# Kernel tuning notes

Hardware: AMD Instinct MI355X
Metric: run time of the kernel (lower is better)

The kernel has to match this reference:

```python
import jax, jax.numpy as jnp
import numpy as np

B, T, DM, DK = 16, 2048, 1024, 128

def setup_inputs() -> dict:
    key = jax.random.key(0)
    k1, k2, k3, k4 = jax.random.split(key, 4)
    x = jax.random.normal(k1, (B, T, DM), dtype=jnp.float32)
    # Linear(dm, dk, bias=False) weights, stored as [dm, dk] for x @ W
    scale = 1.0 / np.sqrt(DM)
    W_q = jax.random.normal(k2, (DM, DK), dtype=jnp.float32) * scale
    W_k = jax.random.normal(k3, (DM, DK), dtype=jnp.float32) * scale
    W_v = jax.random.normal(k4, (DM, DK), dtype=jnp.float32) * scale
    return {"x": x, "W_q": W_q, "W_k": W_k, "W_v": W_v}

def reference(x, W_q, W_k, W_v):
    # q, k, v: [B, T, DK]
    q = jnp.einsum('btd,dk->btk', x, W_q)
    k = jnp.einsum('btd,dk->btk', x, W_k)
    v = jnp.einsum('btd,dk->btk', x, W_v)
    dk = k.shape[-1]
    # scores: [B, T, T], scaled by dk**-0.5
    wei = jnp.einsum('bqk,bsk->bqs', q, k) * (dk ** -0.5)
    # causal mask (tril == 0 -> -inf)
    causal = jnp.tril(jnp.ones((q.shape[1], q.shape[1]), dtype=bool))
    wei = jnp.where(causal, wei, -jnp.inf)
    wei = jax.nn.softmax(wei, axis=-1)
    out = jnp.einsum('bqs,bsk->bqk', wei, v)  # [B, T, DK]
    return out
```

## Files before the change

### kernel.cpp

```cpp
#include <hip/hip_runtime.h>
#include <hip/hip_bf16.h>

#define NB 16
#define NT 2048
#define NDM 1024
#define NDK 128

typedef __bf16 bf16;
typedef bf16 bf16x4 __attribute__((ext_vector_type(4)));
typedef bf16 bf16x8 __attribute__((ext_vector_type(8)));
typedef float f32x4 __attribute__((ext_vector_type(4)));

__device__ inline bf16 to_bf16(float f) {
    __hip_bfloat16 h = __float2bfloat16(f);
    return *reinterpret_cast<bf16*>(&h);
}

__device__ inline void gload_lds16(const void* g, void* l) {
    __builtin_amdgcn_global_load_lds(
        (const __attribute__((address_space(1))) unsigned int*)g,
        (__attribute__((address_space(3))) unsigned int*)l, 16, 0, 0);
}

__global__ __launch_bounds__(256) void transpose_w_kernel(
        const float* __restrict__ Wq, const float* __restrict__ Wk,
        const float* __restrict__ Wv, bf16* __restrict__ Wt) {
    int idx = blockIdx.x * 256 + threadIdx.x;
    int w = idx >> 17;
    int r = idx & (NDM * NDK - 1);
    int k = r >> 7;
    int n = r & (NDK - 1);
    const float* W = (w == 0) ? Wq : ((w == 1) ? Wk : Wv);
    Wt[(size_t)w * NDK * NDM + (size_t)n * NDM + k] = to_bf16(W[(size_t)k * NDK + n]);
}

__global__ __launch_bounds__(512) void proj_fused_kernel(
        const float* __restrict__ x, const bf16* __restrict__ Wt,
        bf16* __restrict__ qkv, bf16* __restrict__ Vt) {
    __shared__ __align__(16) char smem[65536];
    const int tid = threadIdx.x;
    const int lane = tid & 63, wave = tid >> 6;
    const int wr = wave >> 2, wc = wave & 3;
    const int r16 = lane & 15, kg = lane >> 4;
    const int mb = blockIdx.x;
    const float* xA = x + (size_t)mb * 128 * NDM;

    auto ASB = [&](int b) -> bf16* { return (bf16*)(smem + b * 8192); };
    auto BSB = [&](int b) -> bf16* { return (bf16*)(smem + 16384 + b * 24576); };

    const int a_row = tid >> 2, a_c = tid & 3;
    const int a_dst = (a_row * 4 + (a_c ^ ((a_row >> 1) & 3))) * 8;
    const size_t a_src = (size_t)a_row * NDM + a_c * 8;

    auto loadA = [&](int k0, float4& lo, float4& hi) {
        lo = *reinterpret_cast<const float4*>(xA + a_src + k0);
        hi = *reinterpret_cast<const float4*>(xA + a_src + k0 + 4);
    };
    auto writeA = [&](int buf, const float4& lo, const float4& hi) {
        bf16x8 v;
        v[0] = to_bf16(lo.x); v[1] = to_bf16(lo.y); v[2] = to_bf16(lo.z); v[3] = to_bf16(lo.w);
        v[4] = to_bf16(hi.x); v[5] = to_bf16(hi.y); v[6] = to_bf16(hi.z); v[7] = to_bf16(hi.w);
        *reinterpret_cast<bf16x8*>(ASB(buf) + a_dst) = v;
    };
    auto stageB = [&](int buf, int k0) {
#pragma unroll
        for (int p = 0; p < 3; p++) {
            int cid = p * 512 + tid;
            int w = cid >> 9, rem = cid & 511;
            int row = rem >> 2, c = rem & 3;
            int cs = c ^ ((row >> 1) & 3);
            gload_lds16(Wt + (size_t)w * NDK * NDM + (size_t)row * NDM + k0 + cs * 8,
                        BSB(buf) + (p * 512 + wave * 64) * 8);
        }
    };

    f32x4 acc[3][4][2];
#pragma unroll
    for (int w = 0; w < 3; w++)
#pragma unroll
        for (int m = 0; m < 4; m++)
#pragma unroll
            for (int n = 0; n < 2; n++) acc[w][m][n] = (f32x4){0.f, 0.f, 0.f, 0.f};

    {
        float4 lo, hi;
        loadA(0, lo, hi);
        writeA(0, lo, hi);
        stageB(0, 0);
    }
    __syncthreads();

    for (int kt = 0; kt < NDM / 32; kt++) {
        const int cur = kt & 1;
        const bool pf = (kt + 1 < NDM / 32);
        float4 lo, hi;
        if (pf) {
            loadA((kt + 1) * 32, lo, hi);
            stageB(1 - cur, (kt + 1) * 32);
        }

        bf16x8 af[4];
#pragma unroll
        for (int m = 0; m < 4; m++) {
            int arow = wr * 64 + m * 16 + r16;
            int ch = kg ^ ((arow >> 1) & 3);
            af[m] = *reinterpret_cast<const bf16x8*>(ASB(cur) + (arow * 4 + ch) * 8);
        }
#pragma unroll
        for (int w = 0; w < 3; w++) {
#pragma unroll
            for (int n = 0; n < 2; n++) {
                int brow = wc * 32 + n * 16 + r16;
                int ch = kg ^ ((brow >> 1) & 3);
                bf16x8 bfw = *reinterpret_cast<const bf16x8*>(
                    BSB(cur) + ((w * 128 + brow) * 4 + ch) * 8);
#pragma unroll
                for (int m = 0; m < 4; m++)
                    acc[w][m][n] = __builtin_amdgcn_mfma_f32_16x16x32_bf16(af[m], bfw, acc[w][m][n], 0, 0, 0);
            }
        }

        if (pf) writeA(1 - cur, lo, hi);
        __syncthreads();
    }

#pragma unroll
    for (int w = 0; w < 2; w++) {
        bf16* outw = qkv + (size_t)w * (size_t)(NB * NT) * NDK;
#pragma unroll
        for (int m = 0; m < 4; m++) {
            int rowb = mb * 128 + wr * 64 + m * 16 + kg * 4;
#pragma unroll
            for (int n = 0; n < 2; n++) {
                int col = wc * 32 + n * 16 + r16;
#pragma unroll
                for (int r = 0; r < 4; r++)
                    outw[(size_t)(rowb + r) * NDK + col] = to_bf16(acc[w][m][n][r]);
            }
        }
    }
    bf16 (*Tl)[136] = reinterpret_cast<bf16(*)[136]>(smem);
#pragma unroll
    for (int m = 0; m < 4; m++) {
        int tl = wr * 64 + m * 16 + kg * 4;
#pragma unroll
        for (int n = 0; n < 2; n++) {
            int d = wc * 32 + n * 16 + r16;
            bf16x4 pv = { to_bf16(acc[2][m][n][0]), to_bf16(acc[2][m][n][1]),
                          to_bf16(acc[2][m][n][2]), to_bf16(acc[2][m][n][3]) };
            *reinterpret_cast<bf16x4*>(&Tl[d][tl]) = pv;
        }
    }
    __syncthreads();
    const int b = mb >> 4;
    const int t0 = (mb & 15) * 128;
    bf16* Vb = Vt + (size_t)b * NDK * NT;
#pragma unroll
    for (int p = 0; p < 4; p++) {
        int idx = p * 512 + tid;
        int d = idx >> 4, c = idx & 15;
        *reinterpret_cast<bf16x8*>(&Vb[(size_t)d * NT + t0 + c * 8]) =
            *reinterpret_cast<const bf16x8*>(&Tl[d][c * 8]);
    }
}

__global__ __launch_bounds__(256) void attn_kernel(
        const bf16* __restrict__ Q, const bf16* __restrict__ K,
        const bf16* __restrict__ Vt, float* __restrict__ out) {
    __shared__ bf16 Ks[2][64][128];
    __shared__ bf16 Vs[2][128][64];
    __shared__ bf16 Ps[4][16][72];
    const int tid = threadIdx.x, lane = tid & 63, wave = tid >> 6;
    const int r16 = lane & 15, kg = lane >> 4;

    const int bid = blockIdx.x;
    const int xcd = bid & 7;
    const int j = bid >> 3;
    const int b = xcd * 2 + (j & 1);
    const int qb = (NT / 64 - 1) - (j >> 1);
    const int q0 = qb * 64;
    const size_t baseB = (size_t)b * NT * NDK;
    const size_t baseVt = (size_t)b * NDK * NT;

    const float scale = 0.08838834764831843f;
    bf16x8 qf[4];
    const int qglob = q0 + wave * 16 + r16;
#pragma unroll
    for (int kc = 0; kc < 4; kc++) {
        bf16x8 raw = *reinterpret_cast<const bf16x8*>(&Q[baseB + (size_t)qglob * NDK + kc * 32 + kg * 8]);
#pragma unroll
        for (int jj = 0; jj < 8; jj++) raw[jj] = to_bf16((float)raw[jj] * scale);
        qf[kc] = raw;
    }

    f32x4 o[8];
#pragma unroll
    for (int n = 0; n < 8; n++) o[n] = (f32x4){0.f, 0.f, 0.f, 0.f};
    float mrun = -INFINITY;
    float lrun = 0.f;

    int krow[4], kcol[4], vrow[4], vcol[4];
#pragma unroll
    for (int i = 0; i < 4; i++) {
        int idx = i * 256 + tid;
        krow[i] = idx >> 4; kcol[i] = idx & 15;
        vrow[i] = idx >> 3; vcol[i] = idx & 7;
    }

    const int nsteps = qb + 1;
    bf16x8 kreg[4], vreg[4];
#pragma unroll
    for (int i = 0; i < 4; i++) {
        kreg[i] = *reinterpret_cast<const bf16x8*>(&K[baseB + (size_t)krow[i] * NDK + kcol[i] * 8]);
        vreg[i] = *reinterpret_cast<const bf16x8*>(&Vt[baseVt + (size_t)vrow[i] * NT + vcol[i] * 8]);
    }
#pragma unroll
    for (int i = 0; i < 4; i++) {
        *reinterpret_cast<bf16x8*>(&Ks[0][krow[i]][(kcol[i] ^ (krow[i] & 7)) * 8]) = kreg[i];
        *reinterpret_cast<bf16x8*>(&Vs[0][vrow[i]][(vcol[i] ^ (vrow[i] & 7)) * 8]) = vreg[i];
    }
    if (nsteps > 1) {
#pragma unroll
        for (int i = 0; i < 4; i++) {
            kreg[i] = *reinterpret_cast<const bf16x8*>(&K[baseB + (size_t)(64 + krow[i]) * NDK + kcol[i] * 8]);
            vreg[i] = *reinterpret_cast<const bf16x8*>(&Vt[baseVt + (size_t)vrow[i] * NT + 64 + vcol[i] * 8]);
        }
    }
    __syncthreads();

    for (int s = 0; s < nsteps; s++) {
        const int cur = s & 1;
        const int kv0 = s * 64;

        f32x4 sfr[4];
#pragma unroll
        for (int n = 0; n < 4; n++) sfr[n] = (f32x4){0.f, 0.f, 0.f, 0.f};
#pragma unroll
        for (int n = 0; n < 4; n++) {
            const int krw = n * 16 + r16;
#pragma unroll
            for (int kc = 0; kc < 4; kc++) {
                bf16x8 kf = *reinterpret_cast<const bf16x8*>(&Ks[cur][krw][((kc * 4 + kg) ^ (krw & 7)) * 8]);
                sfr[n] = __builtin_amdgcn_mfma_f32_16x16x32_bf16(kf, qf[kc], sfr[n], 0, 0, 0);
            }
        }

        if (s == nsteps - 1) {
#pragma unroll
            for (int n = 0; n < 4; n++)
#pragma unroll
                for (int r = 0; r < 4; r++)
                    if (kv0 + n * 16 + kg * 4 + r > qglob) sfr[n][r] = -INFINITY;
        }

        float pm = -INFINITY;
#pragma unroll
        for (int n = 0; n < 4; n++) {
            float t0 = fmaxf(fmaxf(sfr[n][0], sfr[n][1]), fmaxf(sfr[n][2], sfr[n][3]));
            pm = fmaxf(pm, t0);
        }
        pm = fmaxf(pm, __shfl_xor(pm, 16, 64));
        pm = fmaxf(pm, __shfl_xor(pm, 32, 64));

        if (__any(pm > mrun)) {
            float mnew = fmaxf(mrun, pm);
            float corr = __expf(mrun - mnew);
            mrun = mnew;
            lrun *= corr;
            float co[4];
#pragma unroll
            for (int r = 0; r < 4; r++) co[r] = __shfl(corr, kg * 4 + r, 64);
#pragma unroll
            for (int n = 0; n < 8; n++)
#pragma unroll
                for (int r = 0; r < 4; r++) o[n][r] *= co[r];
        }

        float ps = 0.f;
#pragma unroll
        for (int n = 0; n < 4; n++) {
            bf16x4 pw;
#pragma unroll
            for (int r = 0; r < 4; r++) {
                float pv = __expf(sfr[n][r] - mrun);
                ps += pv;
                pw[r] = to_bf16(pv);
            }
            *reinterpret_cast<bf16x4*>(&Ps[wave][r16][n * 16 + kg * 4]) = pw;
        }
        ps += __shfl_xor(ps, 16, 64);
        ps += __shfl_xor(ps, 32, 64);
        lrun += ps;

#pragma unroll
        for (int kc2 = 0; kc2 < 2; kc2++) {
            bf16x8 pf = *reinterpret_cast<const bf16x8*>(&Ps[wave][r16][kc2 * 32 + kg * 8]);
#pragma unroll
            for (int n = 0; n < 8; n++) {
                const int vrw = n * 16 + r16;
                bf16x8 vf = *reinterpret_cast<const bf16x8*>(&Vs[cur][vrw][((kc2 * 4 + kg) ^ (vrw & 7)) * 8]);
                o[n] = __builtin_amdgcn_mfma_f32_16x16x32_bf16(pf, vf, o[n], 0, 0, 0);
            }
        }

        if (s + 1 < nsteps) {
#pragma unroll
            for (int i = 0; i < 4; i++) {
                *reinterpret_cast<bf16x8*>(&Ks[1 - cur][krow[i]][(kcol[i] ^ (krow[i] & 7)) * 8]) = kreg[i];
                *reinterpret_cast<bf16x8*>(&Vs[1 - cur][vrow[i]][(vcol[i] ^ (vrow[i] & 7)) * 8]) = vreg[i];
            }
            if (s + 2 < nsteps) {
                const int kv2 = (s + 2) * 64;
#pragma unroll
                for (int i = 0; i < 4; i++) {
                    kreg[i] = *reinterpret_cast<const bf16x8*>(&K[baseB + (size_t)(kv2 + krow[i]) * NDK + kcol[i] * 8]);
                    vreg[i] = *reinterpret_cast<const bf16x8*>(&Vt[baseVt + (size_t)vrow[i] * NT + kv2 + vcol[i] * 8]);
                }
            }
        }
        __syncthreads();
    }

    float linv = 1.0f / lrun;
    float li[4];
#pragma unroll
    for (int r = 0; r < 4; r++) li[r] = __shfl(linv, kg * 4 + r, 64);
#pragma unroll
    for (int n = 0; n < 8; n++)
#pragma unroll
        for (int r = 0; r < 4; r++) {
            int row = q0 + wave * 16 + kg * 4 + r;
            int col = n * 16 + r16;
            out[baseB + (size_t)row * NDK + col] = o[n][r] * li[r];
        }
}

extern "C" void kernel_launch(void* const* d_in, const int* in_sizes, int n_in,
                              void* d_out, int out_size, void* d_ws, size_t ws_size,
                              hipStream_t stream) {
    const float* x  = (const float*)d_in[0];
    const float* Wq = (const float*)d_in[1];
    const float* Wk = (const float*)d_in[2];
    const float* Wv = (const float*)d_in[3];
    float* out = (float*)d_out;

    char* ws = (char*)d_ws;
    bf16* Wt  = (bf16*)ws;
    bf16* qkv = (bf16*)(ws + (1ull << 20));
    bf16* Vtg = (bf16*)(ws + (26ull << 20));

    transpose_w_kernel<<<(3 * NDM * NDK) / 256, 256, 0, stream>>>(Wq, Wk, Wv, Wt);

    proj_fused_kernel<<<(NB * NT) / 128, 512, 0, stream>>>(x, Wt, qkv, Vtg);

    bf16* Qp = qkv;
    bf16* Kp = qkv + (size_t)(NB * NT) * NDK;

    attn_kernel<<<dim3((NT / 64) * NB), 256, 0, stream>>>(Qp, Kp, Vtg, out);
}
```

Measured before the change: 100.4 us.

## Deepen projection GEMM prefetch to two stages with explicit vmcnt waits

```diff
diff --git a/kernel.cpp b/kernel.cpp
--- a/kernel.cpp
+++ b/kernel.cpp
@@ -21,6 +21,10 @@
         (const __attribute__((address_space(1))) unsigned int*)g,
         (__attribute__((address_space(3))) unsigned int*)l, 16, 0, 0);
 }
+
+#define VMCNT(n) asm volatile("s_waitcnt vmcnt(" #n ")" ::: "memory")
+#define LGKM0()  asm volatile("s_waitcnt lgkmcnt(0)" ::: "memory")
+#define SCHEDB() __builtin_amdgcn_sched_barrier(0)
 
 __global__ __launch_bounds__(256) void transpose_w_kernel(
         const float* __restrict__ Wq, const float* __restrict__ Wk,
@@ -34,7 +38,7 @@
     Wt[(size_t)w * NDK * NDM + (size_t)n * NDM + k] = to_bf16(W[(size_t)k * NDK + n]);
 }
 
-__global__ __launch_bounds__(512) void proj_fused_kernel(
+__global__ __launch_bounds__(512, 2) void proj_fused_kernel(
         const float* __restrict__ x, const bf16* __restrict__ Wt,
         bf16* __restrict__ qkv, bf16* __restrict__ Vt) {
     __shared__ __align__(16) char smem[65536];
@@ -52,25 +56,27 @@
     const int a_dst = (a_row * 4 + (a_c ^ ((a_row >> 1) & 3))) * 8;
     const size_t a_src = (size_t)a_row * NDM + a_c * 8;
 
-    auto loadA = [&](int k0, float4& lo, float4& hi) {
-        lo = *reinterpret_cast<const float4*>(xA + a_src + k0);
-        hi = *reinterpret_cast<const float4*>(xA + a_src + k0 + 4);
+    float4 alo, ahi;
+    auto loadA = [&](int kt) {
+        const float* src = xA + a_src + kt * 32;
+        alo = *reinterpret_cast<const float4*>(src);
+        ahi = *reinterpret_cast<const float4*>(src + 4);
     };
-    auto writeA = [&](int buf, const float4& lo, const float4& hi) {
+    auto writeA = [&](int buf) {
         bf16x8 v;
-        v[0] = to_bf16(lo.x); v[1] = to_bf16(lo.y); v[2] = to_bf16(lo.z); v[3] = to_bf16(lo.w);
-        v[4] = to_bf16(hi.x); v[5] = to_bf16(hi.y); v[6] = to_bf16(hi.z); v[7] = to_bf16(hi.w);
+        v[0] = to_bf16(alo.x); v[1] = to_bf16(alo.y); v[2] = to_bf16(alo.z); v[3] = to_bf16(alo.w);
+        v[4] = to_bf16(ahi.x); v[5] = to_bf16(ahi.y); v[6] = to_bf16(ahi.z); v[7] = to_bf16(ahi.w);
         *reinterpret_cast<bf16x8*>(ASB(buf) + a_dst) = v;
     };
-    auto stageB = [&](int buf, int k0) {
+    auto stageB = [&](int buf, int kt) {
 #pragma unroll
         for (int p = 0; p < 3; p++) {
             int cid = p * 512 + tid;
             int w = cid >> 9, rem = cid & 511;
             int row = rem >> 2, c = rem & 3;
             int cs = c ^ ((row >> 1) & 3);
-            gload_lds16(Wt + (size_t)w * NDK * NDM + (size_t)row * NDM + k0 + cs * 8,
-                        BSB(buf) + (p * 512 + wave * 64) * 8);
+            gload_lds16(Wt + (size_t)w * NDK * NDM + (size_t)row * NDM + kt * 32 + cs * 8,
+                        BSB(buf) + (size_t)(p * 512 + wave * 64) * 8);
         }
     };
 
@@ -82,23 +88,16 @@
 #pragma unroll
             for (int n = 0; n < 2; n++) acc[w][m][n] = (f32x4){0.f, 0.f, 0.f, 0.f};
 
-    {
-        float4 lo, hi;
-        loadA(0, lo, hi);
-        writeA(0, lo, hi);
-        stageB(0, 0);
-    }
-    __syncthreads();
-
-    for (int kt = 0; kt < NDM / 32; kt++) {
+    loadA(0); SCHEDB(); stageB(0, 0); SCHEDB();
+    VMCNT(3);
+    writeA(0);
+    loadA(1); SCHEDB(); stageB(1, 1); SCHEDB();
+    VMCNT(5);
+    LGKM0();
+    __builtin_amdgcn_s_barrier();
+
+    for (int kt = 0; kt < 32; kt++) {
         const int cur = kt & 1;
-        const bool pf = (kt + 1 < NDM / 32);
-        float4 lo, hi;
-        if (pf) {
-            loadA((kt + 1) * 32, lo, hi);
-            stageB(1 - cur, (kt + 1) * 32);
-        }
-
         bf16x8 af[4];
 #pragma unroll
         for (int m = 0; m < 4; m++) {
@@ -120,10 +119,22 @@
             }
         }
 
-        if (pf) writeA(1 - cur, lo, hi);
-        __syncthreads();
-    }
-
+        if (kt + 1 < 32) {
+            VMCNT(3);
+            writeA(1 - cur);
+            LGKM0();
+            __builtin_amdgcn_s_barrier();
+            if (kt + 2 < 32) {
+                loadA(kt + 2); SCHEDB(); stageB(cur, kt + 2); SCHEDB();
+                VMCNT(5);
+            } else {
+                VMCNT(0);
+            }
+        }
+    }
+
+    __syncthreads();
+    bf16 (*Tl)[136] = reinterpret_cast<bf16(*)[136]>(smem);
 #pragma unroll
     for (int w = 0; w < 2; w++) {
         bf16* outw = qkv + (size_t)w * (size_t)(NB * NT) * NDK;
@@ -139,7 +150,6 @@
             }
         }
     }
-    bf16 (*Tl)[136] = reinterpret_cast<bf16(*)[136]>(smem);
 #pragma unroll
     for (int m = 0; m < 4; m++) {
         int tl = wr * 64 + m * 16 + kg * 4;
```

New measurement: 101.5 us. No clear change (+1.1%).
